# Kernel tuning notes

Hardware: AMD Instinct MI355X
Metric: run time of the kernel (lower is better)

## Reference

```python
import jax, jax.numpy as jnp
import numpy as np

VOCAB = 400000
DIM = 128        # meta['embed_dim']
NBITS = 2        # bits per code
CODEBOOK = 1 << NBITS   # 4 codebook entries
MASK = CODEBOOK - 1
N_WORDS = VOCAB * DIM * NBITS // 32  # 3,200,000 packed int32 words


def setup_inputs() -> dict:
    key = jax.random.key(0)
    k1, k2, k3 = jax.random.split(key, 3)
    input_ids = jax.random.randint(k1, (64, 4096), 0, VOCAB, dtype=jnp.int64)
    # packed bit array: nonnegative int32 words (top bit clear so >> is logical)
    bit_arr = jax.random.randint(k2, (N_WORDS,), 0, 2147483647, dtype=jnp.int32)
    codebook = jax.random.normal(k3, (CODEBOOK,), dtype=jnp.float32)
    return {"input": input_ids, "bit_arr": bit_arr, "codebook": codebook}


def reference(input, bit_arr, codebook):
    flat = input.reshape(-1).astype(jnp.int32)            # [N]
    # code position for (token, dim): p = token*DIM + dim
    pos = flat[:, None] * DIM + jnp.arange(DIM, dtype=jnp.int32)[None, :]  # [N, DIM]
    bitpos = pos * NBITS
    word = bitpos >> 5            # // 32
    shift = bitpos & 31           # % 32
    codes = (bit_arr[word] >> shift) & MASK               # [N, DIM] in [0, 2^NBITS)
    embeds = codebook[codes]                              # [N, DIM] fp32
    return embeds.reshape(input.shape + (DIM,))
```

## Files before the change

### kernel.cpp

```cpp
#include <hip/hip_runtime.h>
#include <hip/hip_bf16.h>


#define EMB_DIM 128

__global__ __launch_bounds__(256) void embed2bit_kernel(
    const int* __restrict__ ids,
    const int* __restrict__ bits,
    const float* __restrict__ cb,
    float* __restrict__ out,
    int n_tokens)
{
    int gid = blockIdx.x * blockDim.x + threadIdx.x;
    int t = gid >> 5;
    int k = gid & 31;
    if (t >= n_tokens) return;

    int tok = ids[t];
    int word = bits[tok * 8 + (k >> 2)];
    int byte = (word >> ((k & 3) * 8)) & 0xff;

    float c0 = cb[0], c1 = cb[1], c2 = cb[2], c3 = cb[3];

    float4 r;
    float* rp = &r.x;
#pragma unroll
    for (int j = 0; j < 4; ++j) {
        int c = (byte >> (2 * j)) & 3;
        float lo = (c & 1) ? c1 : c0;
        float hi = (c & 1) ? c3 : c2;
        rp[j] = (c & 2) ? hi : lo;
    }

    *reinterpret_cast<float4*>(out + (size_t)t * EMB_DIM + k * 4) = r;
}

extern "C" void kernel_launch(void* const* d_in, const int* in_sizes, int n_in,
                              void* d_out, int out_size, void* d_ws, size_t ws_size,
                              hipStream_t stream) {
    const int*   ids  = (const int*)d_in[0];
    const int*   bits = (const int*)d_in[1];
    const float* cb   = (const float*)d_in[2];
    float*       out  = (float*)d_out;

    int n_tokens = in_sizes[0];
    long long total_threads = (long long)n_tokens * 32;
    int block = 256;
    int grid = (int)((total_threads + block - 1) / block);

    embed2bit_kernel<<<grid, block, 0, stream>>>(ids, bits, cb, out, n_tokens);
}
```

Measured before the change: 166.7 us.

## Use grid-stride loop with batched loads and nontemporal stores

Replaces the one-thread-per-item launch with a capped grid of 2048 blocks running a grid-stride loop. Each iteration batches four items, issuing their id loads and then their bit-word loads together before computing, which raises memory-level parallelism. Output is written with nontemporal vector stores so the large streaming output does not pollute the cache. The costs are fewer resident waves, extra 64-bit index arithmetic, and a launch-bounds occupancy hint.

```diff
diff --git a/kernel.cpp b/kernel.cpp
--- a/kernel.cpp
+++ b/kernel.cpp
@@ -4,35 +4,55 @@
 
 #define EMB_DIM 128
 
-__global__ __launch_bounds__(256) void embed2bit_kernel(
+typedef float vfloat4 __attribute__((ext_vector_type(4)));
+
+__global__ __launch_bounds__(256, 8) void embed2bit_kernel(
     const int* __restrict__ ids,
     const int* __restrict__ bits,
     const float* __restrict__ cb,
     float* __restrict__ out,
     int n_tokens)
 {
-    int gid = blockIdx.x * blockDim.x + threadIdx.x;
-    int t = gid >> 5;
-    int k = gid & 31;
-    if (t >= n_tokens) return;
-
-    int tok = ids[t];
-    int word = bits[tok * 8 + (k >> 2)];
-    int byte = (word >> ((k & 3) * 8)) & 0xff;
+    const long long n_items = (long long)n_tokens * 32;
+    const long long stride  = (long long)gridDim.x * blockDim.x;
+    long long gid = (long long)blockIdx.x * blockDim.x + threadIdx.x;
 
     float c0 = cb[0], c1 = cb[1], c2 = cb[2], c3 = cb[3];
 
-    float4 r;
-    float* rp = &r.x;
+    for (long long base = gid; base < n_items; base += 4 * stride) {
+        long long idx[4];
+        int tok[4], wrd[4];
+        bool ok[4];
+
 #pragma unroll
-    for (int j = 0; j < 4; ++j) {
-        int c = (byte >> (2 * j)) & 3;
-        float lo = (c & 1) ? c1 : c0;
-        float hi = (c & 1) ? c3 : c2;
-        rp[j] = (c & 2) ? hi : lo;
+        for (int j = 0; j < 4; ++j) {
+            idx[j] = base + (long long)j * stride;
+            ok[j]  = idx[j] < n_items;
+            tok[j] = ok[j] ? ids[idx[j] >> 5] : 0;
+        }
+#pragma unroll
+        for (int j = 0; j < 4; ++j) {
+            int k  = (int)(idx[j] & 31);
+            wrd[j] = ok[j] ? bits[(long long)tok[j] * 8 + (k >> 2)] : 0;
+        }
+#pragma unroll
+        for (int j = 0; j < 4; ++j) {
+            if (!ok[j]) continue;
+            int k    = (int)(idx[j] & 31);
+            int byte = (wrd[j] >> ((k & 3) * 8)) & 0xff;
+            vfloat4 r;
+#pragma unroll
+            for (int q = 0; q < 4; ++q) {
+                int c    = (byte >> (2 * q)) & 3;
+                float lo = (c & 1) ? c1 : c0;
+                float hi = (c & 1) ? c3 : c2;
+                r[q]     = (c & 2) ? hi : lo;
+            }
+            long long t = idx[j] >> 5;
+            __builtin_nontemporal_store(
+                r, reinterpret_cast<vfloat4*>(out + t * EMB_DIM + k * 4));
+        }
     }
-
-    *reinterpret_cast<float4*>(out + (size_t)t * EMB_DIM + k * 4) = r;
 }
 
 extern "C" void kernel_launch(void* const* d_in, const int* in_sizes, int n_in,
@@ -44,9 +64,11 @@
     float*       out  = (float*)d_out;
 
     int n_tokens = in_sizes[0];
-    long long total_threads = (long long)n_tokens * 32;
+    long long n_items = (long long)n_tokens * 32;
+
     int block = 256;
-    int grid = (int)((total_threads + block - 1) / block);
+    long long want = (n_items + block - 1) / block;
+    int grid = (int)(want < 2048 ? want : 2048);
 
     embed2bit_kernel<<<grid, block, 0, stream>>>(ids, bits, cb, out, n_tokens);
 }
```

New measurement: 163.8 us. Within noise of the previous version (-1.8%).

## Split lookup into word-gather kernel and streaming decode kernel via workspace

Applied to the files above, without the earlier changes.

Splits the fused kernel in two. The first kernel gathers the 8 packed words per token into a contiguous workspace buffer, and the second decodes those words into fp32 embeddings with purely sequential reads. A fused fallback runs when the workspace is too small. The aim is to separate the random gather from the large streaming write, at the cost of an extra launch plus a workspace write and read.

```diff
diff --git a/kernel.cpp b/kernel.cpp
--- a/kernel.cpp
+++ b/kernel.cpp
@@ -4,35 +4,64 @@
 
 #define EMB_DIM 128
 
-__global__ __launch_bounds__(256) void embed2bit_kernel(
+__global__ __launch_bounds__(256) void gather_words_kernel(
     const int* __restrict__ ids,
     const int* __restrict__ bits,
+    int* __restrict__ ws_words,
+    int n_words)
+{
+    int i = blockIdx.x * blockDim.x + threadIdx.x;
+    if (i >= n_words) return;
+    int tok = ids[i >> 3];
+    ws_words[i] = bits[tok * 8 + (i & 7)];
+}
+
+__global__ __launch_bounds__(256) void decode_kernel(
+    const int* __restrict__ ws_words,
     const float* __restrict__ cb,
     float* __restrict__ out,
-    int n_tokens)
+    int n_items)
 {
-    int gid = blockIdx.x * blockDim.x + threadIdx.x;
-    int t = gid >> 5;
-    int k = gid & 31;
-    if (t >= n_tokens) return;
+    int i = blockIdx.x * blockDim.x + threadIdx.x;
+    if (i >= n_items) return;
 
-    int tok = ids[t];
-    int word = bits[tok * 8 + (k >> 2)];
-    int byte = (word >> ((k & 3) * 8)) & 0xff;
+    int word = ws_words[i >> 2];
+    int byte = (word >> ((i & 3) * 8)) & 0xff;
 
     float c0 = cb[0], c1 = cb[1], c2 = cb[2], c3 = cb[3];
 
     float4 r;
     float* rp = &r.x;
 #pragma unroll
-    for (int j = 0; j < 4; ++j) {
-        int c = (byte >> (2 * j)) & 3;
+    for (int q = 0; q < 4; ++q) {
+        int c    = (byte >> (2 * q)) & 3;
         float lo = (c & 1) ? c1 : c0;
         float hi = (c & 1) ? c3 : c2;
-        rp[j] = (c & 2) ? hi : lo;
+        rp[q]    = (c & 2) ? hi : lo;
     }
+    *reinterpret_cast<float4*>(out + (size_t)i * 4) = r;
+}
 
-    *reinterpret_cast<float4*>(out + (size_t)t * EMB_DIM + k * 4) = r;
+__global__ __launch_bounds__(256) void fused_kernel(
+    const int* __restrict__ ids, const int* __restrict__ bits,
+    const float* __restrict__ cb, float* __restrict__ out, int n_items)
+{
+    int i = blockIdx.x * blockDim.x + threadIdx.x;
+    if (i >= n_items) return;
+    int t = i >> 5, k = i & 31;
+    int tok  = ids[t];
+    int word = bits[tok * 8 + (k >> 2)];
+    int byte = (word >> ((k & 3) * 8)) & 0xff;
+    float c0 = cb[0], c1 = cb[1], c2 = cb[2], c3 = cb[3];
+    float4 r; float* rp = &r.x;
+#pragma unroll
+    for (int q = 0; q < 4; ++q) {
+        int c = (byte >> (2 * q)) & 3;
+        float lo = (c & 1) ? c1 : c0;
+        float hi = (c & 1) ? c3 : c2;
+        rp[q] = (c & 2) ? hi : lo;
+    }
+    *reinterpret_cast<float4*>(out + (size_t)i * 4) = r;
 }
 
 extern "C" void kernel_launch(void* const* d_in, const int* in_sizes, int n_in,
@@ -44,9 +73,18 @@
     float*       out  = (float*)d_out;
 
     int n_tokens = in_sizes[0];
-    long long total_threads = (long long)n_tokens * 32;
+    int n_words  = n_tokens * 8;
+    int n_items  = n_tokens * 32;
     int block = 256;
-    int grid = (int)((total_threads + block - 1) / block);
 
-    embed2bit_kernel<<<grid, block, 0, stream>>>(ids, bits, cb, out, n_tokens);
+    if (ws_size >= (size_t)n_words * sizeof(int)) {
+        int* ws_words = (int*)d_ws;
+        gather_words_kernel<<<(n_words + block - 1) / block, block, 0, stream>>>(
+            ids, bits, ws_words, n_words);
+        decode_kernel<<<(n_items + block - 1) / block, block, 0, stream>>>(
+            ws_words, cb, out, n_items);
+    } else {
+        fused_kernel<<<(n_items + block - 1) / block, block, 0, stream>>>(
+            ids, bits, cb, out, n_items);
+    }
 }
```

Result: faster. 152.5 us (-8.5%).

## Stage packed code rows in LDS and process 64 tokens per block

Applied to the files above, without the earlier changes.

Each block now handles 64 tokens. 128 threads first load each token's 32-byte packed row as two 16-byte vector loads into shared memory. After a barrier, all 256 threads loop eight times, decoding bytes from LDS and writing float4 outputs. This removes the redundant per-thread id loads and the scattered 4-byte gathers, at the cost of a sync point, fewer blocks, and idle threads during the staging phase.

```diff
diff --git a/kernel.cpp b/kernel.cpp
--- a/kernel.cpp
+++ b/kernel.cpp
@@ -3,36 +3,57 @@
 
 
 #define EMB_DIM 128
+#define TOK_PER_BLOCK 64
+#define BLOCK 256
 
-__global__ __launch_bounds__(256) void embed2bit_kernel(
+typedef float vfloat4 __attribute__((ext_vector_type(4)));
+typedef int   vint4   __attribute__((ext_vector_type(4)));
+
+__global__ __launch_bounds__(BLOCK) void embed2bit_lds_kernel(
     const int* __restrict__ ids,
     const int* __restrict__ bits,
     const float* __restrict__ cb,
     float* __restrict__ out,
     int n_tokens)
 {
-    int gid = blockIdx.x * blockDim.x + threadIdx.x;
-    int t = gid >> 5;
-    int k = gid & 31;
-    if (t >= n_tokens) return;
+    __shared__ int lds_words[TOK_PER_BLOCK * 8];
 
-    int tok = ids[t];
-    int word = bits[tok * 8 + (k >> 2)];
-    int byte = (word >> ((k & 3) * 8)) & 0xff;
+    const int t0  = blockIdx.x * TOK_PER_BLOCK;
+    const int tid = threadIdx.x;
 
-    float c0 = cb[0], c1 = cb[1], c2 = cb[2], c3 = cb[3];
+    if (tid < TOK_PER_BLOCK * 2) {
+        int t = t0 + (tid >> 1);
+        if (t < n_tokens) {
+            int tok = ids[t];
+            vint4 w = *reinterpret_cast<const vint4*>(
+                bits + (long long)tok * 8 + (tid & 1) * 4);
+            *reinterpret_cast<vint4*>(&lds_words[tid * 4]) = w;
+        }
+    }
+    __syncthreads();
 
-    float4 r;
-    float* rp = &r.x;
+    const float c0 = cb[0], c1 = cb[1], c2 = cb[2], c3 = cb[3];
+    const long long out_base = (long long)t0 * EMB_DIM;
+    const int n_items = (n_tokens - t0 >= TOK_PER_BLOCK
+                             ? TOK_PER_BLOCK : n_tokens - t0) * 32;
+
 #pragma unroll
-    for (int j = 0; j < 4; ++j) {
-        int c = (byte >> (2 * j)) & 3;
-        float lo = (c & 1) ? c1 : c0;
-        float hi = (c & 1) ? c3 : c2;
-        rp[j] = (c & 2) ? hi : lo;
+    for (int q = 0; q < 8; ++q) {
+        int item = q * BLOCK + tid;
+        if (item >= n_items) break;
+        int word = lds_words[item >> 2];
+        int byte = (word >> ((item & 3) * 8)) & 0xff;
+
+        vfloat4 r;
+#pragma unroll
+        for (int j = 0; j < 4; ++j) {
+            int c    = (byte >> (2 * j)) & 3;
+            float lo = (c & 1) ? c1 : c0;
+            float hi = (c & 1) ? c3 : c2;
+            r[j]     = (c & 2) ? hi : lo;
+        }
+        *reinterpret_cast<vfloat4*>(out + out_base + (long long)item * 4) = r;
     }
-
-    *reinterpret_cast<float4*>(out + (size_t)t * EMB_DIM + k * 4) = r;
 }
 
 extern "C" void kernel_launch(void* const* d_in, const int* in_sizes, int n_in,
@@ -44,9 +65,7 @@
     float*       out  = (float*)d_out;
 
     int n_tokens = in_sizes[0];
-    long long total_threads = (long long)n_tokens * 32;
-    int block = 256;
-    int grid = (int)((total_threads + block - 1) / block);
+    int grid = (n_tokens + TOK_PER_BLOCK - 1) / TOK_PER_BLOCK;
 
-    embed2bit_kernel<<<grid, block, 0, stream>>>(ids, bits, cb, out, n_tokens);
+    embed2bit_lds_kernel<<<grid, BLOCK, 0, stream>>>(ids, bits, cb, out, n_tokens);
 }
```

Result: faster. 150.3 us, median of 2 (-9.9%).
